# Kernel tuning notes

Measured on AMD Instinct MI355X. Metric: run time of the kernel, lower is better.

Reference implementation:

```python
import jax, jax.numpy as jnp
import numpy as np

HEADS = 16
HEAD_DIM = 64  # embed_size // heads = 1024 // 16


def setup_inputs() -> dict:
    key = jax.random.key(0)
    ks = jax.random.split(key, 9)
    N, Sq, E, C = 4, 2048, 1024, 512
    Skv = 2 * Sq  # keys/values seq must equal doubled query seq (see view trick)
    return {
        "values": jax.random.normal(ks[0], (N, Skv, E), dtype=jnp.float32),
        "keys": jax.random.normal(ks[1], (N, Skv, E), dtype=jnp.float32),
        "queries": jax.random.normal(ks[2], (N, Sq, E), dtype=jnp.float32),
        "mask": jax.random.randint(ks[3], (N, Skv, HEADS, HEADS), 0, 2, dtype=jnp.int32),
        "condition": jax.random.normal(ks[4], (N, Sq, C), dtype=jnp.float32),
        "Wc": jax.random.normal(ks[5], (E, C), dtype=jnp.float32) * 0.02,
        "bc": jax.random.normal(ks[6], (E,), dtype=jnp.float32) * 0.02,
        "Wo": jax.random.normal(ks[7], (E, E), dtype=jnp.float32) * 0.02,
        "bo": jax.random.normal(ks[8], (E,), dtype=jnp.float32) * 0.02,
    }


def reference(values, keys, queries, mask, condition, Wc, bc, Wo, bo):
    N = queries.shape[0]
    H, D = HEADS, HEAD_DIM
    # condition_linear + concat: (N, Sq, 2E) -> view doubles seq -> (N, 2Sq, H, D)
    cond_feat = jnp.einsum('nsc,ec->nse', condition, Wc) + bc
    cq = jnp.concatenate([queries, cond_feat], axis=-1).reshape(N, -1, H, D)
    k = keys.reshape(N, -1, H, D)    # (N, 2Sq, H, D)
    v = values.reshape(N, -1, H, D)  # (N, 2Sq, H, D)
    # per-(batch,seq) heads-by-heads attention, exactly as the torch matmul does
    att = jnp.einsum('nshd,nsed->nshe', cq, k) / jnp.sqrt(jnp.float32(D))
    att = jnp.where(mask == 0, jnp.float32(-1e20), att)
    att = jax.nn.softmax(att, axis=-1)
    out = jnp.einsum('nshe,nsed->nshd', att, v).reshape(N, -1, H * D)
    return jnp.einsum('nsk,ek->nse', out, Wo) + bo
```

## Files before the change

### kernel.cpp

```cpp
#include <hip/hip_runtime.h>
#include <hip/hip_bf16.h>
#include <type_traits>

#define NB   4
#define SQ   2048
#define SKV  4096
#define EMB  1024
#define CDIM 512

typedef __attribute__((ext_vector_type(8))) short short8;
typedef __attribute__((ext_vector_type(4))) float f32x4;

__device__ __forceinline__ float b2f(ushort u) {
    union { unsigned int i; float f; } v;
    v.i = ((unsigned int)u) << 16;
    return v.f;
}
__device__ __forceinline__ ushort f2b(float f) {
    union { float f; unsigned int i; } v; v.f = f;
    unsigned int x = v.i;
    return (ushort)((x + 0x7fffu + ((x >> 16) & 1u)) >> 16);
}

__device__ __forceinline__ void glds16(const ushort* gp, ushort* lp) {
    __builtin_amdgcn_global_load_lds(
        (const __attribute__((address_space(1))) unsigned int*)gp,
        (__attribute__((address_space(3))) unsigned int*)lp,
        16, 0, 0);
}

__global__ __launch_bounds__(256)
void cvt_f32_bf16(const float* __restrict__ in, ushort* __restrict__ out, int n4)
{
    const int i = blockIdx.x * 256 + threadIdx.x;
    if (i < n4) {
        float4 v = ((const float4*)in)[i];
        ushort4 o;
        o.x = f2b(v.x); o.y = f2b(v.y); o.z = f2b(v.z); o.w = f2b(v.w);
        ((ushort4*)out)[i] = o;
    }
}

template <typename OT>
__global__ __launch_bounds__(256)
void gemm_bt_bias(const ushort* __restrict__ A, const ushort* __restrict__ B,
                  const float* __restrict__ bias, OT* __restrict__ C,
                  int M, int Nn, int K)
{
    __shared__ __attribute__((aligned(16))) ushort As[128 * 32];
    __shared__ __attribute__((aligned(16))) ushort Bs[128 * 32];

    const int tid  = threadIdx.x;
    const int wave = tid >> 6;
    const int lane = tid & 63;
    const int quad = lane >> 4;
    const int l16  = lane & 15;
    const int wr   = wave >> 1;
    const int wc   = wave & 1;

    const long mBase = (long)blockIdx.x * 128;
    const long nBase = (long)blockIdx.y * 128;

    const ushort* Ablk = A + mBase * K;
    const ushort* Bblk = B + nBase * K;

    const int lr = lane >> 2;
    const int lc = (lane & 3) * 8;
    const int c0 = wave * 2, c1 = wave * 2 + 1;
    const ushort* aG0 = Ablk + (long)(c0 * 16 + lr) * K + lc;
    const ushort* aG1 = Ablk + (long)(c1 * 16 + lr) * K + lc;
    const ushort* bG0 = Bblk + (long)(c0 * 16 + lr) * K + lc;
    const ushort* bG1 = Bblk + (long)(c1 * 16 + lr) * K + lc;
    ushort* aL0 = As + c0 * 512;
    ushort* aL1 = As + c1 * 512;
    ushort* bL0 = Bs + c0 * 512;
    ushort* bL1 = Bs + c1 * 512;

    f32x4 acc[4][4];
#pragma unroll
    for (int i = 0; i < 4; ++i)
#pragma unroll
        for (int j = 0; j < 4; ++j)
            acc[i][j] = (f32x4){0.f, 0.f, 0.f, 0.f};

    for (int k0 = 0; k0 < K; k0 += 32) {
        __syncthreads();
        glds16(aG0 + k0, aL0);
        glds16(aG1 + k0, aL1);
        glds16(bG0 + k0, bL0);
        glds16(bG1 + k0, bL1);
        __syncthreads();

        short8 af[4], bfr[4];
#pragma unroll
        for (int mt = 0; mt < 4; ++mt)
            af[mt] = *(const short8*)(As + (wr * 64 + mt * 16 + l16) * 32 + quad * 8);
#pragma unroll
        for (int nt = 0; nt < 4; ++nt)
            bfr[nt] = *(const short8*)(Bs + (wc * 64 + nt * 16 + l16) * 32 + quad * 8);

#pragma unroll
        for (int mt = 0; mt < 4; ++mt)
#pragma unroll
            for (int nt = 0; nt < 4; ++nt)
                acc[mt][nt] = __builtin_amdgcn_mfma_f32_16x16x32_bf16(
                    af[mt], bfr[nt], acc[mt][nt], 0, 0, 0);
    }

#pragma unroll
    for (int mt = 0; mt < 4; ++mt) {
#pragma unroll
        for (int nt = 0; nt < 4; ++nt) {
            const long n = nBase + wc * 64 + nt * 16 + l16;
            const float bv = bias[n];
#pragma unroll
            for (int r = 0; r < 4; ++r) {
                const long m = mBase + wr * 64 + mt * 16 + quad * 4 + r;
                if constexpr (std::is_same<OT, float>::value)
                    C[m * Nn + n] = acc[mt][nt][r] + bv;
                else
                    C[m * Nn + n] = f2b(acc[mt][nt][r] + bv);
            }
        }
    }
}

__global__ __launch_bounds__(256)
void attn_kernel(const float*  __restrict__ queries,
                 const ushort* __restrict__ condfeat,
                 const float*  __restrict__ keys,
                 const float*  __restrict__ values,
                 const int*    __restrict__ mask,
                 ushort* __restrict__ attout)
{
    const int pos = blockIdx.x;
    const int s2  = pos & 4095;
    const int n   = pos >> 12;
    const int tid = threadIdx.x;

    __shared__ __attribute__((aligned(16))) float cq[16 * 68];
    __shared__ __attribute__((aligned(16))) float ks[16 * 68];
    __shared__ __attribute__((aligned(16))) float vs[16 * 68];
    __shared__ float sc[16 * 17];

    {
        const int base = tid * 4;
        const int h = base >> 6, d = base & 63;
        float4 q4;
        if (s2 & 1) {
            const ushort* cp = condfeat + ((size_t)n * SQ + (s2 >> 1)) * EMB + base;
            ushort4 c4 = *(const ushort4*)cp;
            q4.x = b2f(c4.x); q4.y = b2f(c4.y); q4.z = b2f(c4.z); q4.w = b2f(c4.w);
        } else {
            q4 = *(const float4*)(queries + ((size_t)n * SQ + (s2 >> 1)) * EMB + base);
        }
        float4 k4 = *(const float4*)(keys   + (size_t)pos * EMB + base);
        float4 v4 = *(const float4*)(values + (size_t)pos * EMB + base);
        *(float4*)(cq + h * 68 + d) = q4;
        *(float4*)(ks + h * 68 + d) = k4;
        *(float4*)(vs + h * 68 + d) = v4;
    }
    __syncthreads();

    {
        const int h = tid >> 4, e = tid & 15;
        float s = 0.f;
#pragma unroll
        for (int d = 0; d < 64; d += 4) {
            float4 a = *(const float4*)(cq + h * 68 + d);
            float4 b = *(const float4*)(ks + e * 68 + d);
            s += a.x * b.x + a.y * b.y + a.z * b.z + a.w * b.w;
        }
        s *= 0.125f;
        const int mv = mask[(size_t)pos * 256 + tid];
        s = (mv == 0) ? -1e20f : s;

        float mx = s;
#pragma unroll
        for (int d = 1; d < 16; d <<= 1)
            mx = fmaxf(mx, __shfl_xor(mx, d));
        const float ex = __expf(s - mx);
        float sum = ex;
#pragma unroll
        for (int d = 1; d < 16; d <<= 1)
            sum += __shfl_xor(sum, d);
        sc[h * 17 + e] = ex / sum;
    }
    __syncthreads();

    {
        const int idx = tid * 4;
        const int h = idx >> 6, d0 = idx & 63;
        float4 a = {0.f, 0.f, 0.f, 0.f};
#pragma unroll
        for (int e = 0; e < 16; ++e) {
            const float p = sc[h * 17 + e];
            float4 v4 = *(const float4*)(vs + e * 68 + d0);
            a.x += p * v4.x; a.y += p * v4.y; a.z += p * v4.z; a.w += p * v4.w;
        }
        ushort4 o;
        o.x = f2b(a.x); o.y = f2b(a.y); o.z = f2b(a.z); o.w = f2b(a.w);
        *(ushort4*)(attout + (size_t)pos * EMB + idx) = o;
    }
}

extern "C" void kernel_launch(void* const* d_in, const int* in_sizes, int n_in,
                              void* d_out, int out_size, void* d_ws, size_t ws_size,
                              hipStream_t stream)
{
    const float* values    = (const float*)d_in[0];
    const float* keys      = (const float*)d_in[1];
    const float* queries   = (const float*)d_in[2];
    const int*   mask      = (const int*)  d_in[3];
    const float* condition = (const float*)d_in[4];
    const float* Wc        = (const float*)d_in[5];
    const float* bc        = (const float*)d_in[6];
    const float* Wo        = (const float*)d_in[7];
    const float* bo        = (const float*)d_in[8];
    float* out = (float*)d_out;

    ushort* condfeat = (ushort*)d_ws;
    ushort* attout   = condfeat + (size_t)NB * SQ * EMB;
    ushort* cond_bf  = attout;
    ushort* Wc_bf    = attout + (size_t)NB * SQ * CDIM;
    ushort* Wo_bf    = condfeat;

    cvt_f32_bf16<<<(NB * SQ * CDIM / 4 + 255) / 256, 256, 0, stream>>>(
        condition, cond_bf, NB * SQ * CDIM / 4);
    cvt_f32_bf16<<<(EMB * CDIM / 4 + 255) / 256, 256, 0, stream>>>(
        Wc, Wc_bf, EMB * CDIM / 4);

    {
        dim3 grid((NB * SQ) / 128, EMB / 128);
        gemm_bt_bias<ushort><<<grid, 256, 0, stream>>>(
            cond_bf, Wc_bf, bc, condfeat, NB * SQ, EMB, CDIM);
    }

    attn_kernel<<<NB * SKV, 256, 0, stream>>>(queries, condfeat, keys, values,
                                              mask, attout);

    cvt_f32_bf16<<<(EMB * EMB / 4 + 255) / 256, 256, 0, stream>>>(
        Wo, Wo_bf, EMB * EMB / 4);

    {
        dim3 grid((NB * SKV) / 128, EMB / 128);
        gemm_bt_bias<float><<<grid, 256, 0, stream>>>(
            attout, Wo_bf, bo, out, NB * SKV, EMB, EMB);
    }
}
```

Before: 302.7 us.

## Compute per-position head attention with one wave per position using MFMA

```diff
diff --git a/kernel.cpp b/kernel.cpp
--- a/kernel.cpp
+++ b/kernel.cpp
@@ -20,6 +20,12 @@
     union { float f; unsigned int i; } v; v.f = f;
     unsigned int x = v.i;
     return (ushort)((x + 0x7fffu + ((x >> 16) & 1u)) >> 16);
+}
+__device__ __forceinline__ short8 pack_bf16x8(float4 a, float4 b) {
+    union { short8 s; ushort u[8]; } r;
+    r.u[0] = f2b(a.x); r.u[1] = f2b(a.y); r.u[2] = f2b(a.z); r.u[3] = f2b(a.w);
+    r.u[4] = f2b(b.x); r.u[5] = f2b(b.y); r.u[6] = f2b(b.z); r.u[7] = f2b(b.w);
+    return r.s;
 }
 
 __device__ __forceinline__ void glds16(const ushort* gp, ushort* lp) {
@@ -133,48 +139,43 @@
                  const int*    __restrict__ mask,
                  ushort* __restrict__ attout)
 {
-    const int pos = blockIdx.x;
-    const int s2  = pos & 4095;
-    const int n   = pos >> 12;
-    const int tid = threadIdx.x;
-
-    __shared__ __attribute__((aligned(16))) float cq[16 * 68];
-    __shared__ __attribute__((aligned(16))) float ks[16 * 68];
-    __shared__ __attribute__((aligned(16))) float vs[16 * 68];
-    __shared__ float sc[16 * 17];
-
+    const int wid  = threadIdx.x >> 6;
+    const int pos  = blockIdx.x * 4 + wid;
+    const int s2   = pos & 4095;
+    const int n    = pos >> 12;
+    const int lane = threadIdx.x & 63;
+    const int quad = lane >> 4;
+    const int l16  = lane & 15;
+
+    short8 aF[2], bF[2];
+    if (s2 & 1) {
+        const ushort* cp = condfeat + ((size_t)n * SQ + (s2 >> 1)) * EMB
+                           + l16 * 64 + quad * 8;
+        aF[0] = *(const short8*)cp;
+        aF[1] = *(const short8*)(cp + 32);
+    } else {
+        const float* qp = queries + ((size_t)n * SQ + (s2 >> 1)) * EMB
+                          + l16 * 64 + quad * 8;
+        aF[0] = pack_bf16x8(*(const float4*)qp,        *(const float4*)(qp + 4));
+        aF[1] = pack_bf16x8(*(const float4*)(qp + 32), *(const float4*)(qp + 36));
+    }
     {
-        const int base = tid * 4;
-        const int h = base >> 6, d = base & 63;
-        float4 q4;
-        if (s2 & 1) {
-            const ushort* cp = condfeat + ((size_t)n * SQ + (s2 >> 1)) * EMB + base;
-            ushort4 c4 = *(const ushort4*)cp;
-            q4.x = b2f(c4.x); q4.y = b2f(c4.y); q4.z = b2f(c4.z); q4.w = b2f(c4.w);
-        } else {
-            q4 = *(const float4*)(queries + ((size_t)n * SQ + (s2 >> 1)) * EMB + base);
-        }
-        float4 k4 = *(const float4*)(keys   + (size_t)pos * EMB + base);
-        float4 v4 = *(const float4*)(values + (size_t)pos * EMB + base);
-        *(float4*)(cq + h * 68 + d) = q4;
-        *(float4*)(ks + h * 68 + d) = k4;
-        *(float4*)(vs + h * 68 + d) = v4;
-    }
-    __syncthreads();
-
-    {
-        const int h = tid >> 4, e = tid & 15;
-        float s = 0.f;
-#pragma unroll
-        for (int d = 0; d < 64; d += 4) {
-            float4 a = *(const float4*)(cq + h * 68 + d);
-            float4 b = *(const float4*)(ks + e * 68 + d);
-            s += a.x * b.x + a.y * b.y + a.z * b.z + a.w * b.w;
-        }
-        s *= 0.125f;
-        const int mv = mask[(size_t)pos * 256 + tid];
+        const float* kp = keys + (size_t)pos * EMB + l16 * 64 + quad * 8;
+        bF[0] = pack_bf16x8(*(const float4*)kp,        *(const float4*)(kp + 4));
+        bF[1] = pack_bf16x8(*(const float4*)(kp + 32), *(const float4*)(kp + 36));
+    }
+
+    f32x4 sc = (f32x4){0.f, 0.f, 0.f, 0.f};
+    sc = __builtin_amdgcn_mfma_f32_16x16x32_bf16(aF[0], bF[0], sc, 0, 0, 0);
+    sc = __builtin_amdgcn_mfma_f32_16x16x32_bf16(aF[1], bF[1], sc, 0, 0, 0);
+
+    const int* mrow = mask + (size_t)pos * 256;
+    float p[4];
+#pragma unroll
+    for (int r = 0; r < 4; ++r) {
+        float s = sc[r] * 0.125f;
+        const int mv = mrow[(quad * 4 + r) * 16 + l16];
         s = (mv == 0) ? -1e20f : s;
-
         float mx = s;
 #pragma unroll
         for (int d = 1; d < 16; d <<= 1)
@@ -184,23 +185,40 @@
 #pragma unroll
         for (int d = 1; d < 16; d <<= 1)
             sum += __shfl_xor(sum, d);
-        sc[h * 17 + e] = ex / sum;
-    }
-    __syncthreads();
-
-    {
-        const int idx = tid * 4;
-        const int h = idx >> 6, d0 = idx & 63;
-        float4 a = {0.f, 0.f, 0.f, 0.f};
-#pragma unroll
-        for (int e = 0; e < 16; ++e) {
-            const float p = sc[h * 17 + e];
-            float4 v4 = *(const float4*)(vs + e * 68 + d0);
-            a.x += p * v4.x; a.y += p * v4.y; a.z += p * v4.z; a.w += p * v4.w;
+        p[r] = ex / sum;
+    }
+
+    float4 acc[4];
+#pragma unroll
+    for (int r = 0; r < 4; ++r) acc[r] = (float4){0.f, 0.f, 0.f, 0.f};
+
+    const float* vp = values + (size_t)pos * EMB + l16 * 4;
+#pragma unroll
+    for (int eh = 0; eh < 2; ++eh) {
+        float4 vv[8];
+#pragma unroll
+        for (int j = 0; j < 8; ++j)
+            vv[j] = *(const float4*)(vp + (eh * 8 + j) * 64);
+#pragma unroll
+        for (int r = 0; r < 4; ++r) {
+#pragma unroll
+            for (int j = 0; j < 8; ++j) {
+                const float pe = __shfl(p[r], quad * 16 + eh * 8 + j);
+                acc[r].x += pe * vv[j].x;
+                acc[r].y += pe * vv[j].y;
+                acc[r].z += pe * vv[j].z;
+                acc[r].w += pe * vv[j].w;
+            }
         }
+    }
+
+    ushort* op = attout + (size_t)pos * EMB;
+#pragma unroll
+    for (int r = 0; r < 4; ++r) {
         ushort4 o;
-        o.x = f2b(a.x); o.y = f2b(a.y); o.z = f2b(a.z); o.w = f2b(a.w);
-        *(ushort4*)(attout + (size_t)pos * EMB + idx) = o;
+        o.x = f2b(acc[r].x); o.y = f2b(acc[r].y);
+        o.z = f2b(acc[r].z); o.w = f2b(acc[r].w);
+        *(ushort4*)(op + (quad * 4 + r) * 64 + l16 * 4) = o;
     }
 }
 
@@ -236,8 +254,8 @@
             cond_bf, Wc_bf, bc, condfeat, NB * SQ, EMB, CDIM);
     }
 
-    attn_kernel<<<NB * SKV, 256, 0, stream>>>(queries, condfeat, keys, values,
-                                              mask, attout);
+    attn_kernel<<<(NB * SKV) / 4, 256, 0, stream>>>(
+        queries, condfeat, keys, values, mask, attout);
 
     cvt_f32_bf16<<<(EMB * EMB / 4 + 255) / 256, 256, 0, stream>>>(
         Wo, Wo_bf, EMB * EMB / 4);
```

New measurement: 309.2 us. +2.1%, slower.
